# Performance work log

Hardware: AMD Instinct MI355X
Metric: run time of the kernel (lower is better)

Reference implementation:

```python
import jax, jax.numpy as jnp
import numpy as np

TOP_K = 2

def setup_inputs() -> dict:
    key = jax.random.key(0)
    k1, k2, k3, k4 = jax.random.split(key, 4)
    B, T, C = 4, 2048, 1024
    E, D_FF = 8, 1024  # d_ff = 1 * n_embd
    x = jax.random.normal(k1, (B, T, C), dtype=jnp.float32)
    router_w = jax.random.normal(k2, (E, C), dtype=jnp.float32) * 0.02
    w1 = jax.random.normal(k3, (E, C, D_FF), dtype=jnp.float32) * 0.02
    w2 = jax.random.normal(k4, (E, D_FF, C), dtype=jnp.float32) * 0.02
    return {"x": x, "router_w": router_w, "w1": w1, "w2": w2}

def reference(x, router_w, w1, w2):
    B, T, C = x.shape
    x_flat = x.reshape(-1, C)                          # [N, C]
    logits = x_flat @ router_w.T                       # [N, E]
    probs = jax.nn.softmax(logits, axis=-1)
    weights, indices = jax.lax.top_k(probs, TOP_K)     # [N, K], [N, K]
    # Dense per-expert compute (same math as gathering w1/w2 per token,
    # without duplicating weight slices per token).
    hidden = jax.nn.relu(jnp.einsum('nc,ecf->nef', x_flat, w1))  # [N, E, d_ff]
    out_all = jnp.einsum('nef,efc->nec', hidden, w2)             # [N, E, C]
    sel = jnp.take_along_axis(out_all, indices[:, :, None], axis=1)  # [N, K, C]
    out = jnp.sum(sel * weights[:, :, None], axis=1)   # [N, C]
    return out.reshape(B, T, C)
```

## Files before the change

kernel.cpp:

```cpp
#include <hip/hip_runtime.h>
#include <hip/hip_bf16.h>

#define NTOK 8192
#define CDIM 1024
#define FDIM 1024
#define NEXP 8
#define BM 256
#define BN 256
#define BK 64
#define NKT (CDIM / BK)
#define NWG 384

typedef __attribute__((ext_vector_type(8))) short short8;
typedef __attribute__((ext_vector_type(4))) float f32x4;

union Pack4 { __hip_bfloat16 h[4]; unsigned long long v; };
union U4 { unsigned long long u; unsigned short s[4]; };

typedef const unsigned int __attribute__((address_space(1)))* gas_ptr;
typedef unsigned int __attribute__((address_space(3)))* las_ptr;

__device__ __forceinline__ void gload16(const void* g, void* l) {
    __builtin_amdgcn_global_load_lds(
        (gas_ptr)(unsigned long long)g,
        (las_ptr)(unsigned int)(unsigned long long)l,
        16, 0, 0);
}

__device__ __forceinline__ float bf2f(unsigned short v) {
    unsigned int t = (unsigned int)v << 16;
    return __uint_as_float(t);
}

__device__ __forceinline__ bool find_full_tile(const int* __restrict__ cnt, int tIdx,
                                               int& e, int& m0, int& off) {
    int acc = 0, s = 0;
    for (int ee = 0; ee < NEXP; ee++) {
        int me = cnt[ee * 16];
        int nf = me >> 8;
        if (tIdx < acc + nf) { e = ee; m0 = (tIdx - acc) << 8; off = s; return true; }
        acc += nf; s += me;
    }
    return false;
}
__device__ __forceinline__ bool find_fill_tile(const int* __restrict__ cnt, int tIdx,
                                               int& e, int& m0, int& off, int& me_out) {
    int acc = 0, s = 0;
    for (int ee = 0; ee < NEXP; ee++) {
        int me = cnt[ee * 16];
        int base = (me >> 8) << 8;
        int nr = (me - base + 127) >> 7;
        if (tIdx < acc + nr) {
            e = ee; m0 = base + ((tIdx - acc) << 7); off = s; me_out = me; return true;
        }
        acc += nr; s += me;
    }
    return false;
}

struct RouterSh2 {
    float xs[2][16][256];
    int lcnt[NEXP];
    int lt[NEXP][32];
    float lw[NEXP][32];
    int base[NEXP];
};

__global__ __launch_bounds__(256) void router_transpose(
    const float* __restrict__ x, const float* __restrict__ rw,
    __hip_bfloat16* __restrict__ xb,
    int* __restrict__ cnt, int* __restrict__ rows, float* __restrict__ wts,
    int* __restrict__ slotEI,
    const float* __restrict__ w1, const float* __restrict__ w2,
    __hip_bfloat16* __restrict__ w1t, __hip_bfloat16* __restrict__ w2t)
{
    __shared__ alignas(16) char shraw[sizeof(RouterSh2)];
    const int bid = blockIdx.x;
    const int tid = threadIdx.x;

    if (bid < 512) {
        RouterSh2* sh = reinterpret_cast<RouterSh2*>(shraw);
        const int wv = tid >> 6, lane = tid & 63;
        if (tid < NEXP) sh->lcnt[tid] = 0;
        const int n0b = bid * 16;

#pragma unroll
        for (int i = 0; i < 4; i++)
            gload16(x + (size_t)(n0b + i * 4 + wv) * CDIM + lane * 4,
                    (char*)&sh->xs[0][0][0] + i * 4096 + wv * 1024);

        float acc[4][NEXP];
#pragma unroll
        for (int tt = 0; tt < 4; tt++)
#pragma unroll
            for (int e = 0; e < NEXP; e++) acc[tt][e] = 0.f;

        int cur = 0;
        for (int c = 0; c < 4; c++) {
            __builtin_amdgcn_s_barrier();
            if (c + 1 < 4) {
#pragma unroll
                for (int i = 0; i < 4; i++)
                    gload16(x + (size_t)(n0b + i * 4 + wv) * CDIM + (c + 1) * 256 + lane * 4,
                            (char*)&sh->xs[cur ^ 1][0][0] + i * 4096 + wv * 1024);
                asm volatile("s_waitcnt vmcnt(4)" ::: "memory");
            } else {
                asm volatile("s_waitcnt vmcnt(0)" ::: "memory");
            }
            __builtin_amdgcn_s_barrier();
            __builtin_amdgcn_sched_barrier(0);

            float4 w4[NEXP];
#pragma unroll
            for (int e = 0; e < NEXP; e++)
                w4[e] = *(const float4*)&rw[e * CDIM + c * 256 + lane * 4];

#pragma unroll
            for (int tt = 0; tt < 4; tt++) {
                float4 xv = *(const float4*)&sh->xs[cur][wv * 4 + tt][lane * 4];
                Pack4 p4;
                p4.h[0] = __float2bfloat16(xv.x); p4.h[1] = __float2bfloat16(xv.y);
                p4.h[2] = __float2bfloat16(xv.z); p4.h[3] = __float2bfloat16(xv.w);
                *(unsigned long long*)(xb + (size_t)(n0b + wv * 4 + tt) * CDIM
                                       + c * 256 + lane * 4) = p4.v;
#pragma unroll
                for (int e = 0; e < NEXP; e++)
                    acc[tt][e] += xv.x * w4[e].x + xv.y * w4[e].y +
                                  xv.z * w4[e].z + xv.w * w4[e].w;
            }
            cur ^= 1;
        }

#pragma unroll
        for (int tt = 0; tt < 4; tt++)
#pragma unroll
            for (int e = 0; e < NEXP; e++)
#pragma unroll
                for (int s = 32; s > 0; s >>= 1)
                    acc[tt][e] += __shfl_xor(acc[tt][e], s);

        if (lane == 0) {
#pragma unroll
            for (int tt = 0; tt < 4; tt++) {
                const int n = n0b + wv * 4 + tt;
                float mx = acc[tt][0];
#pragma unroll
                for (int e = 1; e < NEXP; e++) mx = fmaxf(mx, acc[tt][e]);
                float p[NEXP], se = 0.f;
#pragma unroll
                for (int e = 0; e < NEXP; e++) { p[e] = __expf(acc[tt][e] - mx); se += p[e]; }
                float inv = 1.f / se;
                int i0 = 0;
#pragma unroll
                for (int e = 1; e < NEXP; e++) if (p[e] > p[i0]) i0 = e;
                int i1 = (i0 == 0) ? 1 : 0;
#pragma unroll
                for (int e = 0; e < NEXP; e++) if (e != i0 && p[e] > p[i1]) i1 = e;
                int p0 = atomicAdd(&sh->lcnt[i0], 1);
                sh->lt[i0][p0] = n;
                sh->lw[i0][p0] = p[i0] * inv;
                int p1 = atomicAdd(&sh->lcnt[i1], 1);
                sh->lt[i1][p1] = n | (1 << 16);
                sh->lw[i1][p1] = p[i1] * inv;
            }
        }
        __syncthreads();
        if (tid < NEXP) sh->base[tid] = atomicAdd(&cnt[tid * 16], sh->lcnt[tid]);
        __syncthreads();
#pragma unroll
        for (int e = 0; e < NEXP; e++) {
            for (int i = tid; i < sh->lcnt[e]; i += 256) {
                int v = sh->lt[e][i];
                rows[e * NTOK + sh->base[e] + i] = v;
                wts [e * NTOK + sh->base[e] + i] = sh->lw[e][i];
                slotEI[2 * (v & 0xFFFF) + (v >> 16)] = (e << 14) | (sh->base[e] + i);
            }
        }
    } else {
        float (*t)[65] = reinterpret_cast<float(*)[65]>(shraw);
        const int zb = bid - 512;
        const int z = zb >> 8;
        const float* src = (z < 8) ? w1 : w2;
        __hip_bfloat16* dst = (z < 8) ? w1t : w2t;
        const int e = z & 7;
        const int r0 = ((zb >> 4) & 15) * 64, c0 = (zb & 15) * 64;
        const int rr = tid >> 4;
        const int cc = (tid & 15) * 4;
#pragma unroll
        for (int j = 0; j < 4; j++) {
            int row = j * 16 + rr;
            float4 v = *(const float4*)(src + ((size_t)e * 1024 + r0 + row) * 1024 + c0 + cc);
            t[row][cc] = v.x; t[row][cc + 1] = v.y; t[row][cc + 2] = v.z; t[row][cc + 3] = v.w;
        }
        __syncthreads();
#pragma unroll
        for (int j = 0; j < 4; j++) {
            int trow = j * 16 + rr;
            Pack4 o;
#pragma unroll
            for (int k = 0; k < 4; k++) o.h[k] = __float2bfloat16(t[cc + k][trow]);
            *(unsigned long long*)(dst + ((size_t)e * 1024 + c0 + trow) * 1024 + r0 + cc) = o.v;
        }
    }
}

struct RouterSh {
    int lcnt[NEXP];
    int lt[NEXP][32];
    float lw[NEXP][32];
    int base[NEXP];
};

__global__ __launch_bounds__(256) void router_kernel(
    const float* __restrict__ x, const float* __restrict__ rw,
    __hip_bfloat16* __restrict__ xb,
    int* __restrict__ cnt, int* __restrict__ rows, float* __restrict__ wts,
    int* __restrict__ slotEI)
{
    __shared__ RouterSh sh;
    const int tid = threadIdx.x;
    const int wv = tid >> 6, lane = tid & 63;
    if (tid < NEXP) sh.lcnt[tid] = 0;
    __syncthreads();
    for (int tt = 0; tt < 4; tt++) {
        const int n = blockIdx.x * 16 + wv * 4 + tt;
        float acc[NEXP];
#pragma unroll
        for (int e = 0; e < NEXP; e++) acc[e] = 0.f;
#pragma unroll
        for (int c0 = 0; c0 < CDIM; c0 += 256) {
            const size_t o = (size_t)n * CDIM + c0 + lane * 4;
            float4 xv = *(const float4*)(x + o);
            Pack4 p4;
            p4.h[0] = __float2bfloat16(xv.x); p4.h[1] = __float2bfloat16(xv.y);
            p4.h[2] = __float2bfloat16(xv.z); p4.h[3] = __float2bfloat16(xv.w);
            *(unsigned long long*)(xb + o) = p4.v;
#pragma unroll
            for (int e = 0; e < NEXP; e++) {
                float4 w4 = *(const float4*)&rw[e * CDIM + c0 + lane * 4];
                acc[e] += xv.x * w4.x + xv.y * w4.y + xv.z * w4.z + xv.w * w4.w;
            }
        }
#pragma unroll
        for (int e = 0; e < NEXP; e++) {
#pragma unroll
            for (int s = 32; s > 0; s >>= 1) acc[e] += __shfl_xor(acc[e], s);
        }
        if (lane == 0) {
            float mx = acc[0];
#pragma unroll
            for (int e = 1; e < NEXP; e++) mx = fmaxf(mx, acc[e]);
            float p[NEXP], se = 0.f;
#pragma unroll
            for (int e = 0; e < NEXP; e++) { p[e] = __expf(acc[e] - mx); se += p[e]; }
            float inv = 1.f / se;
            int i0 = 0;
#pragma unroll
            for (int e = 1; e < NEXP; e++) if (p[e] > p[i0]) i0 = e;
            int i1 = (i0 == 0) ? 1 : 0;
#pragma unroll
            for (int e = 0; e < NEXP; e++) if (e != i0 && p[e] > p[i1]) i1 = e;
            int p0 = atomicAdd(&sh.lcnt[i0], 1);
            sh.lt[i0][p0] = n; sh.lw[i0][p0] = p[i0] * inv;
            int p1 = atomicAdd(&sh.lcnt[i1], 1);
            sh.lt[i1][p1] = n | (1 << 16); sh.lw[i1][p1] = p[i1] * inv;
        }
    }
    __syncthreads();
    if (tid < NEXP) sh.base[tid] = atomicAdd(&cnt[tid * 16], sh.lcnt[tid]);
    __syncthreads();
#pragma unroll
    for (int e = 0; e < NEXP; e++) {
        for (int i = tid; i < sh.lcnt[e]; i += 256) {
            int v = sh.lt[e][i];
            rows[e * NTOK + sh.base[e] + i] = v;
            wts [e * NTOK + sh.base[e] + i] = sh.lw[e][i];
            slotEI[2 * (v & 0xFFFF) + (v >> 16)] = (e << 14) | (sh.base[e] + i);
        }
    }
}

__global__ __launch_bounds__(256) void transpose_conv(
    const float* __restrict__ src, __hip_bfloat16* __restrict__ dst)
{
    __shared__ float t[64][65];
    const int e = blockIdx.z;
    const int r0 = blockIdx.x * 64, c0 = blockIdx.y * 64;
    const int tid = threadIdx.x;
    const int rr = tid >> 4;
    const int cc = (tid & 15) * 4;
#pragma unroll
    for (int j = 0; j < 4; j++) {
        int row = j * 16 + rr;
        float4 v = *(const float4*)(src + ((size_t)e * 1024 + r0 + row) * 1024 + c0 + cc);
        t[row][cc] = v.x; t[row][cc + 1] = v.y; t[row][cc + 2] = v.z; t[row][cc + 3] = v.w;
    }
    __syncthreads();
#pragma unroll
    for (int j = 0; j < 4; j++) {
        int trow = j * 16 + rr;
        Pack4 o;
#pragma unroll
        for (int k = 0; k < 4; k++) o.h[k] = __float2bfloat16(t[cc + k][trow]);
        *(unsigned long long*)(dst + ((size_t)e * 1024 + c0 + trow) * 1024 + r0 + cc) = o.v;
    }
}

#define STAGE_A(buf, h, kt) { \
    gload16(asrc[2*(h)]   + (kt)*BK, &smem[buf][0][((2*(h))*512   + wv*64)*8]); \
    gload16(asrc[2*(h)+1] + (kt)*BK, &smem[buf][0][((2*(h)+1)*512 + wv*64)*8]); }
#define STAGE_B(buf, h, kt) { \
    gload16(bsrc[2*(h)]   + (kt)*BK, &smem[buf][1][((2*(h))*512   + wv*64)*8]); \
    gload16(bsrc[2*(h)+1] + (kt)*BK, &smem[buf][1][((2*(h)+1)*512 + wv*64)*8]); }
#define PH_READ_A(buf, mh, ks) { \
    const int cs_ = (((ks)*4 + fq) ^ fx) * 8; \
    _Pragma("unroll") \
    for (int i_ = 0; i_ < 4; i_++) \
        af[i_] = *(const short8*)&smem[buf][0][(wr*128 + (mh)*64 + i_*16 + fr)*64 + cs_]; }
#define PH_READ_B(buf, ks) { \
    const int cs_ = (((ks)*4 + fq) ^ fx) * 8; \
    _Pragma("unroll") \
    for (int n_ = 0; n_ < 4; n_++) \
        bfv[n_] = *(const short8*)&smem[buf][1][(wc*64 + n_*16 + fr)*64 + cs_]; }
#define PH_MFMA(mh) { \
    __builtin_amdgcn_s_setprio(1); \
    _Pragma("unroll") \
    for (int i_ = 0; i_ < 4; i_++) \
        _Pragma("unroll") \
        for (int n_ = 0; n_ < 4; n_++) \
            acc[(mh)*4 + i_][n_] = __builtin_amdgcn_mfma_f32_16x16x32_bf16( \
                af[i_], bfv[n_], acc[(mh)*4 + i_][n_], 0, 0, 0); \
    __builtin_amdgcn_s_setprio(0); }
#define SBAR { \
    __builtin_amdgcn_sched_barrier(0); \
    __builtin_amdgcn_s_barrier(); \
    __builtin_amdgcn_sched_barrier(0); }

#define KLOOP_8PHASE \
    STAGE_A(0, 0, 0); STAGE_A(0, 1, 0); STAGE_B(0, 0, 0); STAGE_B(0, 1, 0); \
    STAGE_B(1, 0, 1); STAGE_B(1, 1, 1); \
    asm volatile("s_waitcnt vmcnt(4)" ::: "memory"); \
    SBAR; \
    _Pragma("unroll 1") \
    for (int j = 0; j < NKT / 2; j++) { \
        const int t2 = 2 * j; \
        const bool full = (j < NKT / 2 - 1); \
        short8 af[4], bfv[4]; \
         \
        PH_READ_A(0, 0, 0); PH_READ_B(0, 0); \
        STAGE_A(1, 0, t2 + 1); STAGE_A(1, 1, t2 + 1); \
        SBAR; PH_MFMA(0); \
         \
        PH_READ_A(0, 1, 0); \
        SBAR; PH_MFMA(1); \
         \
        PH_READ_A(0, 0, 1); PH_READ_B(0, 1); \
        SBAR; PH_MFMA(0); \
         \
        PH_READ_A(0, 1, 1); \
        if (full) { \
            STAGE_B(0, 0, t2 + 2); STAGE_B(0, 1, t2 + 2); \
            asm volatile("s_waitcnt vmcnt(4)" ::: "memory"); \
        } else { \
            asm volatile("s_waitcnt vmcnt(0)" ::: "memory"); \
        } \
        SBAR; PH_MFMA(1); \
         \
        PH_READ_A(1, 0, 0); PH_READ_B(1, 0); \
        if (full) { STAGE_A(0, 0, t2 + 2); STAGE_A(0, 1, t2 + 2); } \
        SBAR; PH_MFMA(0); \
         \
        PH_READ_A(1, 1, 0); \
        SBAR; PH_MFMA(1); \
         \
        PH_READ_A(1, 0, 1); PH_READ_B(1, 1); \
        SBAR; PH_MFMA(0); \
         \
        PH_READ_A(1, 1, 1); \
        if (full) { \
            STAGE_B(1, 0, t2 + 3); STAGE_B(1, 1, t2 + 3); \
            asm volatile("s_waitcnt vmcnt(4)" ::: "memory"); \
        } \
        SBAR; PH_MFMA(1); \
    }

__global__ __launch_bounds__(512, 1) void moe_gemm1(
    const __hip_bfloat16* __restrict__ xb, const __hip_bfloat16* __restrict__ w1t,
    const int* __restrict__ cnt, const int* __restrict__ rows,
    __hip_bfloat16* __restrict__ hid)
{
    const int bid = blockIdx.x;
    const int tid = threadIdx.x;
    const int lane = tid & 63, wv = tid >> 6;
    const int fr = lane & 15, fq = lane >> 4;
    const int fx = fr & 7;

    __shared__ alignas(16) __hip_bfloat16 smem[2][2][BM * BK];

    const int swz8 = (((tid & 7) ^ ((tid >> 3) & 7))) * 8;

    if (bid < 256) {
        const int wid = (bid & 7) * 32 + (bid >> 3);
        const int t = wid >> 2;
        int e, m0, off;
        if (!find_full_tile(cnt, t, e, m0, off)) return;
        const int n0 = (wid & 3) * BN;
        const int wr = wv >> 2, wc = wv & 3;

        const __hip_bfloat16* asrc[4];
        const __hip_bfloat16* bsrc[4];
#pragma unroll
        for (int i = 0; i < 4; i++) {
            int row = i * 64 + (tid >> 3);
            int tok = rows[e * NTOK + m0 + row] & 0xFFFF;
            asrc[i] = xb + (size_t)tok * CDIM + swz8;
            bsrc[i] = w1t + ((size_t)e * FDIM + n0 + row) * CDIM + swz8;
        }

        f32x4 acc[8][4] = {};
        KLOOP_8PHASE;
        __syncthreads();

        __hip_bfloat16 (*Cl)[BN] = reinterpret_cast<__hip_bfloat16(*)[BN]>(&smem[0][0][0]);
#pragma unroll
        for (int m = 0; m < 8; m++)
#pragma unroll
            for (int n = 0; n < 4; n++)
#pragma unroll
                for (int r = 0; r < 4; r++) {
                    int il = wr * 128 + m * 16 + fq * 4 + r;
                    float v = acc[m][n][r];
                    Cl[il][wc * 64 + n * 16 + fr] = __float2bfloat16(v > 0.f ? v : 0.f);
                }
        __syncthreads();
#pragma unroll
        for (int i = 0; i < 16; i++) {
            int chunk = i * 512 + tid;
            int row = chunk >> 5, c8 = (chunk & 31) * 8;
            *(short8*)(hid + (size_t)(off + m0 + row) * FDIM + n0 + c8) =
                *(const short8*)&Cl[row][c8];
        }
    } else {
        const int f = bid - 256;
        const int t = f >> 3;
        int e, m0, off, me;
        if (!find_fill_tile(cnt, t, e, m0, off, me)) return;
        const int n0 = (f & 7) * 128;
        const int wr2 = wv >> 2, wc2 = wv & 3;

        const __hip_bfloat16* asrcF[2];
        const __hip_bfloat16* bsrcF[2];
#pragma unroll
        for (int i = 0; i < 2; i++) {
            int row = i * 64 + (tid >> 3);
            int gi = m0 + row;
            int ri = gi < me ? gi : me - 1;
            int tok = rows[e * NTOK + ri] & 0xFFFF;
            asrcF[i] = xb + (size_t)tok * CDIM + swz8;
            bsrcF[i] = w1t + ((size_t)e * FDIM + n0 + row) * CDIM + swz8;
        }

        f32x4 accF[4][2] = {};

#pragma unroll
        for (int i = 0; i < 2; i++) {
            gload16(asrcF[i], &smem[0][0][(i * 512 + wv * 64) * 8]);
            gload16(bsrcF[i], &smem[0][1][(i * 512 + wv * 64) * 8]);
        }

        int cur = 0;
        for (int kt = 0; kt < NKT; kt++) {
            __builtin_amdgcn_s_barrier();
            if (kt + 1 < NKT) {
                const int k1 = (kt + 1) * BK;
#pragma unroll
                for (int i = 0; i < 2; i++) {
                    gload16(asrcF[i] + k1, &smem[cur ^ 1][0][(i * 512 + wv * 64) * 8]);
                    gload16(bsrcF[i] + k1, &smem[cur ^ 1][1][(i * 512 + wv * 64) * 8]);
                }
                asm volatile("s_waitcnt vmcnt(4)" ::: "memory");
            } else {
                asm volatile("s_waitcnt vmcnt(0)" ::: "memory");
            }
            __builtin_amdgcn_s_barrier();
            __builtin_amdgcn_sched_barrier(0);
#pragma unroll
            for (int ks = 0; ks < 2; ks++) {
                short8 afF[4], bfF[2];
                const int cs = ((ks * 4 + fq) ^ fx) * 8;
#pragma unroll
                for (int m = 0; m < 4; m++)
                    afF[m] = *(const short8*)&smem[cur][0][(wr2 * 64 + m * 16 + fr) * 64 + cs];
#pragma unroll
                for (int n = 0; n < 2; n++)
                    bfF[n] = *(const short8*)&smem[cur][1][(wc2 * 32 + n * 16 + fr) * 64 + cs];
#pragma unroll
                for (int m = 0; m < 4; m++)
#pragma unroll
                    for (int n = 0; n < 2; n++)
                        accF[m][n] = __builtin_amdgcn_mfma_f32_16x16x32_bf16(
                            afF[m], bfF[n], accF[m][n], 0, 0, 0);
            }
            cur ^= 1;
        }
        __syncthreads();

        __hip_bfloat16 (*Cl)[128] = reinterpret_cast<__hip_bfloat16(*)[128]>(&smem[0][0][0]);
#pragma unroll
        for (int m = 0; m < 4; m++)
#pragma unroll
            for (int n = 0; n < 2; n++)
#pragma unroll
                for (int r = 0; r < 4; r++) {
                    int il = wr2 * 64 + m * 16 + fq * 4 + r;
                    float v = accF[m][n][r];
                    Cl[il][wc2 * 32 + n * 16 + fr] = __float2bfloat16(v > 0.f ? v : 0.f);
                }
        __syncthreads();
#pragma unroll
        for (int i = 0; i < 4; i++) {
            int chunk = i * 512 + tid;
            int row = chunk >> 4, c8 = (chunk & 15) * 8;
            int gi = m0 + row;
            if (gi < me)
                *(short8*)(hid + (size_t)(off + gi) * FDIM + n0 + c8) =
                    *(const short8*)&Cl[row][c8];
        }
    }
}

__global__ __launch_bounds__(512, 1) void moe_gemm2(
    const __hip_bfloat16* __restrict__ hid, const __hip_bfloat16* __restrict__ w2t,
    const int* __restrict__ cnt, const int* __restrict__ rows,
    const float* __restrict__ wts, __hip_bfloat16* __restrict__ ybuf,
    float* __restrict__ out)
{
    const int bid = blockIdx.x;
    const int tid = threadIdx.x;
    const int lane = tid & 63, wv = tid >> 6;
    const int fr = lane & 15, fq = lane >> 4;
    const int fx = fr & 7;

    __shared__ alignas(16) __hip_bfloat16 smem[2][2][BM * BK];
    __shared__ int rtok[BM];
    __shared__ float rwt[BM];

    const int swz8 = (((tid & 7) ^ ((tid >> 3) & 7))) * 8;

    if (bid < 256) {
        const int wid = (bid & 7) * 32 + (bid >> 3);
        const int t = wid >> 2;
        int e, m0, off;
        if (!find_full_tile(cnt, t, e, m0, off)) return;
        const int n0 = (wid & 3) * BN;
        const int wr = wv >> 2, wc = wv & 3;

        if (tid < BM) {
            rtok[tid] = rows[e * NTOK + m0 + tid] & 0xFFFF;
            rwt[tid] = wts[e * NTOK + m0 + tid];
        }
        __syncthreads();

        const __hip_bfloat16* asrc[4];
        const __hip_bfloat16* bsrc[4];
#pragma unroll
        for (int i = 0; i < 4; i++) {
            int row = i * 64 + (tid >> 3);
            asrc[i] = hid + (size_t)(off + m0 + row) * FDIM + swz8;
            bsrc[i] = w2t + ((size_t)e * CDIM + n0 + row) * FDIM + swz8;
        }

        f32x4 acc[8][4] = {};
        KLOOP_8PHASE;
        __syncthreads();

        if (ybuf) {
            __hip_bfloat16 (*Cl)[BN] = reinterpret_cast<__hip_bfloat16(*)[BN]>(&smem[0][0][0]);
#pragma unroll
            for (int m = 0; m < 8; m++)
#pragma unroll
                for (int n = 0; n < 4; n++)
#pragma unroll
                    for (int r = 0; r < 4; r++) {
                        int il = wr * 128 + m * 16 + fq * 4 + r;
                        Cl[il][wc * 64 + n * 16 + fr] =
                            __float2bfloat16(rwt[il] * acc[m][n][r]);
                    }
            __syncthreads();
#pragma unroll
            for (int i = 0; i < 16; i++) {
                int chunk = i * 512 + tid;
                int row = chunk >> 5, c8 = (chunk & 31) * 8;
                *(short8*)(ybuf + (size_t)(off + m0 + row) * CDIM + n0 + c8) =
                    *(const short8*)&Cl[row][c8];
            }
        } else {
#pragma unroll
            for (int m = 0; m < 8; m++)
#pragma unroll
                for (int n = 0; n < 4; n++)
#pragma unroll
                    for (int r = 0; r < 4; r++) {
                        int il = wr * 128 + m * 16 + fq * 4 + r;
                        atomicAdd(&out[(size_t)rtok[il] * CDIM + n0 + wc * 64 + n * 16 + fr],
                                  rwt[il] * acc[m][n][r]);
                    }
        }
    } else {
        const int f = bid - 256;
        const int t = f >> 3;
        int e, m0, off, me;
        if (!find_fill_tile(cnt, t, e, m0, off, me)) return;
        const int n0 = (f & 7) * 128;
        const int wr2 = wv >> 2, wc2 = wv & 3;

        if (tid < 128) {
            int gi = m0 + tid;
            int ri = gi < me ? gi : me - 1;
            rtok[tid] = rows[e * NTOK + ri] & 0xFFFF;
            rwt[tid] = gi < me ? wts[e * NTOK + ri] : 0.f;
        }
        __syncthreads();

        const __hip_bfloat16* asrcF[2];
        const __hip_bfloat16* bsrcF[2];
#pragma unroll
        for (int i = 0; i < 2; i++) {
            int row = i * 64 + (tid >> 3);
            int gi = m0 + row;
            int ri = gi < me ? gi : me - 1;
            asrcF[i] = hid + (size_t)(off + ri) * FDIM + swz8;
            bsrcF[i] = w2t + ((size_t)e * CDIM + n0 + row) * FDIM + swz8;
        }

        f32x4 accF[4][2] = {};

#pragma unroll
        for (int i = 0; i < 2; i++) {
            gload16(asrcF[i], &smem[0][0][(i * 512 + wv * 64) * 8]);
            gload16(bsrcF[i], &smem[0][1][(i * 512 + wv * 64) * 8]);
        }

        int cur = 0;
        for (int kt = 0; kt < NKT; kt++) {
            __builtin_amdgcn_s_barrier();
            if (kt + 1 < NKT) {
                const int k1 = (kt + 1) * BK;
#pragma unroll
                for (int i = 0; i < 2; i++) {
                    gload16(asrcF[i] + k1, &smem[cur ^ 1][0][(i * 512 + wv * 64) * 8]);
                    gload16(bsrcF[i] + k1, &smem[cur ^ 1][1][(i * 512 + wv * 64) * 8]);
                }
                asm volatile("s_waitcnt vmcnt(4)" ::: "memory");
            } else {
                asm volatile("s_waitcnt vmcnt(0)" ::: "memory");
            }
            __builtin_amdgcn_s_barrier();
            __builtin_amdgcn_sched_barrier(0);
#pragma unroll
            for (int ks = 0; ks < 2; ks++) {
                short8 afF[4], bfF[2];
                const int cs = ((ks * 4 + fq) ^ fx) * 8;
#pragma unroll
                for (int m = 0; m < 4; m++)
                    afF[m] = *(const short8*)&smem[cur][0][(wr2 * 64 + m * 16 + fr) * 64 + cs];
#pragma unroll
                for (int n = 0; n < 2; n++)
                    bfF[n] = *(const short8*)&smem[cur][1][(wc2 * 32 + n * 16 + fr) * 64 + cs];
#pragma unroll
                for (int m = 0; m < 4; m++)
#pragma unroll
                    for (int n = 0; n < 2; n++)
                        accF[m][n] = __builtin_amdgcn_mfma_f32_16x16x32_bf16(
                            afF[m], bfF[n], accF[m][n], 0, 0, 0);
            }
            cur ^= 1;
        }
        __syncthreads();

        if (ybuf) {
            __hip_bfloat16 (*Cl)[128] = reinterpret_cast<__hip_bfloat16(*)[128]>(&smem[0][0][0]);
#pragma unroll
            for (int m = 0; m < 4; m++)
#pragma unroll
                for (int n = 0; n < 2; n++)
#pragma unroll
                    for (int r = 0; r < 4; r++) {
                        int il = wr2 * 64 + m * 16 + fq * 4 + r;
                        Cl[il][wc2 * 32 + n * 16 + fr] =
                            __float2bfloat16(rwt[il] * accF[m][n][r]);
                    }
            __syncthreads();
#pragma unroll
            for (int i = 0; i < 4; i++) {
                int chunk = i * 512 + tid;
                int row = chunk >> 4, c8 = (chunk & 15) * 8;
                int gi = m0 + row;
                if (gi < me)
                    *(short8*)(ybuf + (size_t)(off + gi) * CDIM + n0 + c8) =
                        *(const short8*)&Cl[row][c8];
            }
        } else {
#pragma unroll
            for (int m = 0; m < 4; m++)
#pragma unroll
                for (int n = 0; n < 2; n++)
#pragma unroll
                    for (int r = 0; r < 4; r++) {
                        int il = wr2 * 64 + m * 16 + fq * 4 + r;
                        int gi = m0 + il;
                        if (gi < me)
                            atomicAdd(&out[(size_t)rtok[il] * CDIM + n0 + wc2 * 32 + n * 16 + fr],
                                      rwt[il] * accF[m][n][r]);
                    }
        }
    }
}

__global__ __launch_bounds__(256) void gather_out(
    const __hip_bfloat16* __restrict__ yb, const int* __restrict__ slotEI,
    const int* __restrict__ cnt, float* __restrict__ out)
{
    for (int n = blockIdx.x; n < NTOK; n += gridDim.x) {
        const int v0 = slotEI[2 * n], v1 = slotEI[2 * n + 1];
        int e0 = v0 >> 14, e1 = v1 >> 14;
        int s0 = v0 & 0x3FFF, s1 = v1 & 0x3FFF;
        for (int ee = 0; ee < NEXP; ee++) {
            int me = cnt[ee * 16];
            if (ee < e0) s0 += me;
            if (ee < e1) s1 += me;
        }
        const int c = threadIdx.x * 4;
        U4 a, b;
        a.u = *(const unsigned long long*)(yb + (size_t)s0 * CDIM + c);
        b.u = *(const unsigned long long*)(yb + (size_t)s1 * CDIM + c);
        float4 o;
        o.x = bf2f(a.s[0]) + bf2f(b.s[0]);
        o.y = bf2f(a.s[1]) + bf2f(b.s[1]);
        o.z = bf2f(a.s[2]) + bf2f(b.s[2]);
        o.w = bf2f(a.s[3]) + bf2f(b.s[3]);
        *(float4*)(out + (size_t)n * CDIM + c) = o;
    }
}

extern "C" void kernel_launch(void* const* d_in, const int* in_sizes, int n_in,
                              void* d_out, int out_size, void* d_ws, size_t ws_size,
                              hipStream_t stream)
{
    const float* x  = (const float*)d_in[0];
    const float* rw = (const float*)d_in[1];
    const float* w1 = (const float*)d_in[2];
    const float* w2 = (const float*)d_in[3];
    float* out = (float*)d_out;
    char* ws = (char*)d_ws;

    int* cnt  = (int*)ws;
    int* rows = (int*)(ws + 4096);
    float* wts = (float*)(ws + 4096 + NEXP * NTOK * 4);
    int* slotEI = (int*)(ws + 4096 + 2 * NEXP * NTOK * 4);

    hipMemsetAsync(cnt, 0, 1024, stream);

    const bool big = ws_size >= ((size_t)81 << 20);
    if (big) {
        __hip_bfloat16* xb  = (__hip_bfloat16*)(ws + (1u << 20));
        __hip_bfloat16* w1t = (__hip_bfloat16*)(ws + (17u << 20));
        __hip_bfloat16* w2t = (__hip_bfloat16*)(ws + (33u << 20));
        __hip_bfloat16* hid = (__hip_bfloat16*)(ws + (49u << 20));
        __hip_bfloat16* ybuf = (__hip_bfloat16*)(ws + (1u << 20));

        router_transpose<<<512 + 4096, 256, 0, stream>>>(
            x, rw, xb, cnt, rows, wts, slotEI, w1, w2, w1t, w2t);
        moe_gemm1<<<NWG, 512, 0, stream>>>(xb, w1t, cnt, rows, hid);
        moe_gemm2<<<NWG, 512, 0, stream>>>(hid, w2t, cnt, rows, wts, ybuf, out);
        gather_out<<<2048, 256, 0, stream>>>(ybuf, slotEI, cnt, out);
    } else {
        __hip_bfloat16* xb  = (__hip_bfloat16*)(ws + (1u << 20));
        __hip_bfloat16* w1t = (__hip_bfloat16*)(ws + (17u << 20));
        __hip_bfloat16* hid = (__hip_bfloat16*)(ws + (33u << 20));
        __hip_bfloat16* w2t = w1t;

        hipMemsetAsync(d_out, 0, (size_t)out_size * sizeof(float), stream);
        router_kernel<<<NTOK / 16, 256, 0, stream>>>(x, rw, xb, cnt, rows, wts, slotEI);
        transpose_conv<<<dim3(16, 16, NEXP), 256, 0, stream>>>(w1, w1t);
        moe_gemm1<<<NWG, 512, 0, stream>>>(xb, w1t, cnt, rows, hid);
        transpose_conv<<<dim3(16, 16, NEXP), 256, 0, stream>>>(w2, w2t);
        moe_gemm2<<<NWG, 512, 0, stream>>>(hid, w2t, cnt, rows, wts, nullptr, out);
    }
}
```

Baseline: 137.1 us.

## Restructure GEMM K-loop from 8-phase to 4-phase schedule with larger MFMA batches

The MoE GEMM main loop now uses four barrier-separated phases per pair of K tiles instead of eight. Each phase reads all 8 A fragments and 4 B fragments and issues 32 MFMAs. A and B tiles for the next buffer are staged together, with different vmcnt waits. This halves the barrier count and enlarges each MFMA batch. In exchange it needs more live fragment registers and makes load/compute interleaving coarser, which could expose global-load latency.

New measurement: 138.6 us. About the same (+1.1%).

```diff
diff --git a/kernel.cpp b/kernel.cpp
--- a/kernel.cpp
+++ b/kernel.cpp
@@ -312,76 +312,61 @@
 #define STAGE_B(buf, h, kt) { \
     gload16(bsrc[2*(h)]   + (kt)*BK, &smem[buf][1][((2*(h))*512   + wv*64)*8]); \
     gload16(bsrc[2*(h)+1] + (kt)*BK, &smem[buf][1][((2*(h)+1)*512 + wv*64)*8]); }
-#define PH_READ_A(buf, mh, ks) { \
+#define RD_A8(buf, ks) { \
     const int cs_ = (((ks)*4 + fq) ^ fx) * 8; \
     _Pragma("unroll") \
-    for (int i_ = 0; i_ < 4; i_++) \
-        af[i_] = *(const short8*)&smem[buf][0][(wr*128 + (mh)*64 + i_*16 + fr)*64 + cs_]; }
-#define PH_READ_B(buf, ks) { \
+    for (int i_ = 0; i_ < 8; i_++) \
+        af[i_] = *(const short8*)&smem[buf][0][(wr*128 + i_*16 + fr)*64 + cs_]; }
+#define RD_B4(buf, ks) { \
     const int cs_ = (((ks)*4 + fq) ^ fx) * 8; \
     _Pragma("unroll") \
     for (int n_ = 0; n_ < 4; n_++) \
         bfv[n_] = *(const short8*)&smem[buf][1][(wc*64 + n_*16 + fr)*64 + cs_]; }
-#define PH_MFMA(mh) { \
+#define MFMA32 { \
     __builtin_amdgcn_s_setprio(1); \
     _Pragma("unroll") \
-    for (int i_ = 0; i_ < 4; i_++) \
+    for (int i_ = 0; i_ < 8; i_++) \
         _Pragma("unroll") \
         for (int n_ = 0; n_ < 4; n_++) \
-            acc[(mh)*4 + i_][n_] = __builtin_amdgcn_mfma_f32_16x16x32_bf16( \
-                af[i_], bfv[n_], acc[(mh)*4 + i_][n_], 0, 0, 0); \
+            acc[i_][n_] = __builtin_amdgcn_mfma_f32_16x16x32_bf16( \
+                af[i_], bfv[n_], acc[i_][n_], 0, 0, 0); \
     __builtin_amdgcn_s_setprio(0); }
-#define SBAR { \
-    __builtin_amdgcn_sched_barrier(0); \
+#define SBART { \
     __builtin_amdgcn_s_barrier(); \
     __builtin_amdgcn_sched_barrier(0); }
 
-#define KLOOP_8PHASE \
+#define KLOOP_4PHASE \
     STAGE_A(0, 0, 0); STAGE_A(0, 1, 0); STAGE_B(0, 0, 0); STAGE_B(0, 1, 0); \
-    STAGE_B(1, 0, 1); STAGE_B(1, 1, 1); \
-    asm volatile("s_waitcnt vmcnt(4)" ::: "memory"); \
-    SBAR; \
+    asm volatile("s_waitcnt vmcnt(0)" ::: "memory"); \
+    SBART; \
     _Pragma("unroll 1") \
     for (int j = 0; j < NKT / 2; j++) { \
         const int t2 = 2 * j; \
         const bool full = (j < NKT / 2 - 1); \
-        short8 af[4], bfv[4]; \
+        short8 af[8], bfv[4]; \
          \
-        PH_READ_A(0, 0, 0); PH_READ_B(0, 0); \
+        RD_A8(0, 0); RD_B4(0, 0); \
         STAGE_A(1, 0, t2 + 1); STAGE_A(1, 1, t2 + 1); \
-        SBAR; PH_MFMA(0); \
+        STAGE_B(1, 0, t2 + 1); STAGE_B(1, 1, t2 + 1); \
+        SBART; MFMA32; \
          \
-        PH_READ_A(0, 1, 0); \
-        SBAR; PH_MFMA(1); \
+        RD_A8(0, 1); RD_B4(0, 1); \
+        SBART; MFMA32; \
          \
-        PH_READ_A(0, 0, 1); PH_READ_B(0, 1); \
-        SBAR; PH_MFMA(0); \
-         \
-        PH_READ_A(0, 1, 1); \
         if (full) { \
+            STAGE_A(0, 0, t2 + 2); STAGE_A(0, 1, t2 + 2); \
             STAGE_B(0, 0, t2 + 2); STAGE_B(0, 1, t2 + 2); \
-            asm volatile("s_waitcnt vmcnt(4)" ::: "memory"); \
+            asm volatile("s_waitcnt vmcnt(8)" ::: "memory"); \
         } else { \
             asm volatile("s_waitcnt vmcnt(0)" ::: "memory"); \
         } \
-        SBAR; PH_MFMA(1); \
+        SBART; \
+        RD_A8(1, 0); RD_B4(1, 0); \
+        MFMA32; \
          \
-        PH_READ_A(1, 0, 0); PH_READ_B(1, 0); \
-        if (full) { STAGE_A(0, 0, t2 + 2); STAGE_A(0, 1, t2 + 2); } \
-        SBAR; PH_MFMA(0); \
-         \
-        PH_READ_A(1, 1, 0); \
-        SBAR; PH_MFMA(1); \
-         \
-        PH_READ_A(1, 0, 1); PH_READ_B(1, 1); \
-        SBAR; PH_MFMA(0); \
-         \
-        PH_READ_A(1, 1, 1); \
-        if (full) { \
-            STAGE_B(1, 0, t2 + 3); STAGE_B(1, 1, t2 + 3); \
-            asm volatile("s_waitcnt vmcnt(4)" ::: "memory"); \
-        } \
-        SBAR; PH_MFMA(1); \
+        RD_A8(1, 1); RD_B4(1, 1); \
+        if (full) { asm volatile("s_waitcnt vmcnt(0)" ::: "memory"); } \
+        SBART; MFMA32; \
     }
 
 __global__ __launch_bounds__(512, 1) void moe_gemm1(
@@ -418,7 +403,7 @@
         }
 
         f32x4 acc[8][4] = {};
-        KLOOP_8PHASE;
+        KLOOP_4PHASE;
         __syncthreads();
 
         __hip_bfloat16 (*Cl)[BN] = reinterpret_cast<__hip_bfloat16(*)[BN]>(&smem[0][0][0]);
@@ -571,7 +556,7 @@
         }
 
         f32x4 acc[8][4] = {};
-        KLOOP_8PHASE;
+        KLOOP_4PHASE;
         __syncthreads();
 
         if (ybuf) {
```
